# Kernel tuning notes

Measured on AMD Instinct MI355X. Metric: run time of the kernel, lower is better.

Reference implementation:

```python
import jax, jax.numpy as jnp
import numpy as np
import math

D_MODEL = 2048
NUM_HEADS = 32
NUM_KV_HEADS = 8
D_K = D_MODEL // NUM_HEADS  # 64
GROUPS = NUM_HEADS // NUM_KV_HEADS  # 4
WINDOW = 512
ROPE_BASE = 10000.0


def setup_inputs() -> dict:
    key = jax.random.key(0)
    ks = jax.random.split(key, 5)
    B, T = 2, 2048
    x = jax.random.normal(ks[0], (B, T, D_MODEL), dtype=jnp.float32)
    s = 0.02  # typical init scale to keep logits sane
    Wq = jax.random.normal(ks[1], (D_MODEL, D_MODEL), dtype=jnp.float32) * s
    Wk = jax.random.normal(ks[2], (NUM_KV_HEADS * D_K, D_MODEL), dtype=jnp.float32) * s
    Wv = jax.random.normal(ks[3], (NUM_KV_HEADS * D_K, D_MODEL), dtype=jnp.float32) * s
    Wo = jax.random.normal(ks[4], (D_MODEL, D_MODEL), dtype=jnp.float32) * s
    return {"x": x, "Wq": Wq, "Wk": Wk, "Wv": Wv, "Wo": Wo}


def _rotate_half(t):
    half = t.shape[-1] // 2
    return jnp.concatenate([-t[..., half:], t[..., :half]], axis=-1)


def _rope_cos_sin(T, dtype):
    inv_freq = 1.0 / (ROPE_BASE ** (jnp.arange(0, D_K, 2, dtype=jnp.float32) / D_K))
    pos = jnp.arange(T, dtype=jnp.float32)
    freqs = pos[:, None] * inv_freq[None, :]            # [T, D_K/2]
    emb = jnp.concatenate([freqs, freqs], axis=-1)       # [T, D_K]
    return jnp.cos(emb).astype(dtype)[None, None], jnp.sin(emb).astype(dtype)[None, None]


def reference(x, Wq, Wk, Wv, Wo):
    B, T, D = x.shape
    # Projections (nn.Linear: x @ W.T)
    Q = (x @ Wq.T).reshape(B, T, NUM_HEADS, D_K).transpose(0, 2, 1, 3)     # [B,H,T,dk]
    K = (x @ Wk.T).reshape(B, T, NUM_KV_HEADS, D_K).transpose(0, 2, 1, 3)  # [B,KV,T,dk]
    V = (x @ Wv.T).reshape(B, T, NUM_KV_HEADS, D_K).transpose(0, 2, 1, 3)
    # RoPE
    cos, sin = _rope_cos_sin(T, x.dtype)
    Q = Q * cos + _rotate_half(Q) * sin
    K = K * cos + _rotate_half(K) * sin
    # GQA: fold group dim into Q instead of repeat_interleave on K/V (same math)
    Qg = Q.reshape(B, NUM_KV_HEADS, GROUPS, T, D_K)
    scale = math.sqrt(D_K)
    scores = jnp.einsum('bhgqd,bhkd->bhgqk', Qg, K) / scale  # [B,KV,G,T,T]
    # sliding-window causal mask: valid iff 0 <= q_pos - k_pos < WINDOW
    pos = jnp.arange(T)
    dist = pos[:, None] - pos[None, :]
    win_mask = (dist < 0) | (dist >= WINDOW)
    scores = jnp.where(win_mask[None, None, None], -jnp.inf, scores)
    attn = jax.nn.softmax(scores, axis=-1)
    out = jnp.einsum('bhgqk,bhkd->bhgqd', attn, V)
    out = out.reshape(B, NUM_HEADS, T, D_K).transpose(0, 2, 1, 3).reshape(B, T, D)
    return out @ Wo.T
```

## Files before the change

kernel.cpp:

```cpp
#include <hip/hip_runtime.h>
#include <hip/hip_bf16.h>
#include <cstdint>
#include <cstddef>

typedef __attribute__((ext_vector_type(4))) float f32x4;
typedef __attribute__((ext_vector_type(8))) short bf16x8;
typedef __attribute__((ext_vector_type(4))) int i32x4;
typedef void __attribute__((address_space(1)))* as1_void_p;
typedef void __attribute__((address_space(3)))* as3_void_p;

#define T_SEQ 2048
#define D_MODEL 2048
#define NUM_HEADS 32
#define NUM_KV 8
#define GROUPS 4
#define DK 64
#define WINDOW 512
#define BATCH 2

#define NEG_BIG (-30000.0f)

__device__ __forceinline__ unsigned short f2b(float f) {
    unsigned int u = __builtin_bit_cast(unsigned int, f);
    u = (u + 0x7FFFu + ((u >> 16) & 1u)) >> 16;
    return (unsigned short)u;
}

__device__ __forceinline__ unsigned int cvtpk_bf16(float lo, float hi) {
    unsigned int r;
    asm("v_cvt_pk_bf16_f32 %0, %1, %2" : "=v"(r) : "v"(lo), "v"(hi));
    return r;
}

__device__ __forceinline__ void load_lds16(const void* g, void* l) {
    __builtin_amdgcn_global_load_lds((as1_void_p)(uintptr_t)g,
                                     (as3_void_p)(unsigned int)(uintptr_t)l,
                                     16, 0, 0);
}

#define CAST_N0 8388608
#define CAST_N1 12582912
#define CAST_N2 13631488
#define CAST_N3 14680064
#define CAST_N4 18874368
__global__ void cast_all_kernel(const float* __restrict__ x, const float* __restrict__ wq,
                                const float* __restrict__ wk, const float* __restrict__ wv,
                                const float* __restrict__ wo, unsigned short* __restrict__ dst) {
    int i = (blockIdx.x * blockDim.x + threadIdx.x) * 4;
    const int stride = gridDim.x * blockDim.x * 4;
    for (; i < CAST_N4; i += stride) {
        const float* src;
        int off;
        if (i < CAST_N0)      { src = x;  off = i; }
        else if (i < CAST_N1) { src = wq; off = i - CAST_N0; }
        else if (i < CAST_N2) { src = wk; off = i - CAST_N1; }
        else if (i < CAST_N3) { src = wv; off = i - CAST_N2; }
        else                  { src = wo; off = i - CAST_N3; }
        const float4 v = *(const float4*)(src + off);
        ushort4 o;
        o.x = f2b(v.x); o.y = f2b(v.y); o.z = f2b(v.z); o.w = f2b(v.w);
        *(ushort4*)(dst + i) = o;
    }
}

__global__ void rope_table_kernel(float* __restrict__ ct, float* __restrict__ st) {
    int i = blockIdx.x * blockDim.x + threadIdx.x;
    int t = i >> 5, j = i & 31;
    const float kln = 0.28782313662425556f;
    float inv = __expf(-(float)j * kln);
    if (j == 0) inv = 1.0f;
    float ang = (float)t * inv;
    float s, c;
    sincosf(ang, &s, &c);
    ct[i] = c; st[i] = s;
}


__global__ __launch_bounds__(512, 4) void gemm_qkv_rope(
    const unsigned short* __restrict__ A, const unsigned short* __restrict__ Bw,
    const float* __restrict__ ct, const float* __restrict__ st,
    unsigned short* __restrict__ Qb, unsigned short* __restrict__ Kb,
    unsigned short* __restrict__ Vt) {
    __shared__ __align__(16) unsigned short lds[32768];
    const int tid = threadIdx.x;
    const int lane = tid & 63;
    const int wid = tid >> 6;
    const int wr = wid >> 1, wc = wid & 1;
    const int lrow = lane & 15;
    const int g = lane >> 4;
    const int tile_m = blockIdx.y, tile_n = blockIdx.x;
    const int arow = tile_m * 128, brow = tile_n * 128;

    const int srow = tid >> 2, sslot = tid & 3;
    const int scol = (sslot ^ ((srow >> 1) & 3)) << 3;

    f32x4 acc[2][4] = {};

#define QSTAGE(BUF, KCOL)                                                      \
    {                                                                          \
        load_lds16(A + (size_t)(arow + srow) * 2048 + (KCOL) + scol,           \
                   (char*)&lds[(BUF) * 8192] + tid * 16);                      \
        load_lds16(Bw + (size_t)(brow + srow) * 2048 + (KCOL) + scol,          \
                   (char*)&lds[(BUF) * 8192 + 4096] + tid * 16);               \
    }

    QSTAGE(0, 0) QSTAGE(1, 32) QSTAGE(2, 64)
    asm volatile("s_waitcnt vmcnt(4)" ::: "memory");
    __builtin_amdgcn_sched_barrier(0);
    __builtin_amdgcn_s_barrier();

    for (int t = 0; t < 64; ++t) {
        const int cb = (t & 3) * 8192;
        const int sb = (t + 3) & 3;
        bf16x8 af[2], bfr[4];
#pragma unroll
        for (int m = 0; m < 2; ++m) {
            const int R = wr * 32 + m * 16 + lrow;
            af[m] = *(const bf16x8*)&lds[cb + R * 32 + ((g ^ ((R >> 1) & 3)) << 3)];
        }
#pragma unroll
        for (int n = 0; n < 4; ++n) {
            const int R = wc * 64 + n * 16 + lrow;
            bfr[n] = *(const bf16x8*)&lds[cb + 4096 + R * 32 + ((g ^ ((R >> 1) & 3)) << 3)];
        }
        if (t + 3 < 64) QSTAGE(sb, (t + 3) * 32)
        __builtin_amdgcn_s_barrier();
        asm volatile("s_waitcnt lgkmcnt(0)" ::: "memory");
        __builtin_amdgcn_sched_barrier(0);
        __builtin_amdgcn_s_setprio(1);
#pragma unroll
        for (int m = 0; m < 2; ++m)
#pragma unroll
            for (int n = 0; n < 4; ++n)
                acc[m][n] = __builtin_amdgcn_mfma_f32_16x16x32_bf16(af[m], bfr[n], acc[m][n], 0, 0, 0);
        __builtin_amdgcn_s_setprio(0);
        if (t < 63) { asm volatile("s_waitcnt vmcnt(4)" ::: "memory"); }
        else        { asm volatile("s_waitcnt vmcnt(0)" ::: "memory"); }
        __builtin_amdgcn_sched_barrier(0);
        __builtin_amdgcn_s_barrier();
    }
#undef QSTAGE

    const int hcol = tile_n * 2 + wc;
#pragma unroll
    for (int m = 0; m < 2; ++m) {
        const int row0 = tile_m * 128 + wr * 32 + m * 16 + g * 4;
        const int bb = row0 >> 11;
        const int t0 = row0 & 2047;
        if (hcol < 40) {
            const bool isQ = (hcol < 32);
            const float sc = isQ ? 0.125f : 1.0f;
            unsigned short* base = isQ
                ? (Qb + ((size_t)(bb * NUM_HEADS + hcol) * T_SEQ) * 64)
                : (Kb + ((size_t)(bb * NUM_KV + (hcol - 32)) * T_SEQ) * 64);
#pragma unroll
            for (int r = 0; r < 4; ++r) {
                const int t = t0 + r;
                unsigned short* dst = base + (size_t)t * 64;
#pragma unroll
                for (int n = 0; n < 2; ++n) {
                    const int j = n * 16 + lrow;
                    const float c = ct[t * 32 + j], s = st[t * 32 + j];
                    const float v0 = acc[m][n][r], v1 = acc[m][n + 2][r];
                    dst[j]      = f2b((v0 * c - v1 * s) * sc);
                    dst[j + 32] = f2b((v1 * c + v0 * s) * sc);
                }
            }
        } else {
            const int vh = hcol - 40;
            const int chunk = t0 >> 5, tk = t0 & 31;
            unsigned short* cbase = Vt + ((size_t)(bb * NUM_KV + vh) * 64 + chunk) * 2048 + tk;
#pragma unroll
            for (int n = 0; n < 4; ++n) {
                const int d = n * 16 + lrow;
                unsigned int u0 = cvtpk_bf16(acc[m][n][0], acc[m][n][1]);
                unsigned int u1 = cvtpk_bf16(acc[m][n][2], acc[m][n][3]);
                uint2 val; val.x = u0; val.y = u1;
                *(uint2*)(cbase + d * 32) = val;
            }
        }
    }
}

__global__ __launch_bounds__(512, 2) void gemm_bf16_nt(
    const unsigned short* __restrict__ A, const unsigned short* __restrict__ B,
    float* __restrict__ C) {
    __shared__ __align__(16) unsigned short lds[49152];
    const int tid = threadIdx.x;
    const int lane = tid & 63;
    const int wid = tid >> 6;
    const int wr = wid >> 2, wc = wid & 3;
    const int lrow = lane & 15;
    const int g = lane >> 4;
    const int tile_m = blockIdx.y, tile_n = blockIdx.x;
    const int arow = tile_m * 128, brow = tile_n * 256;

    const int srow = tid >> 2, sslot = tid & 3;
    const int scol = (sslot ^ ((srow >> 1) & 3)) << 3;

    f32x4 acc[4][4] = {};

#define OSTAGE(BUF, KCOL)                                                      \
    {                                                                          \
        load_lds16(A + (size_t)(arow + srow) * 2048 + (KCOL) + scol,           \
                   (char*)&lds[(BUF) * 12288] + tid * 16);                     \
        _Pragma("unroll") for (int u = 0; u < 2; ++u) {                        \
            const int gi = u * 512 + tid;                                      \
            const int br_ = gi >> 2, bs_ = gi & 3;                             \
            const int bc_ = (bs_ ^ ((br_ >> 1) & 3)) << 3;                     \
            load_lds16(B + (size_t)(brow + br_) * 2048 + (KCOL) + bc_,         \
                       (char*)&lds[(BUF) * 12288 + 4096] + gi * 16);           \
        }                                                                      \
    }

    OSTAGE(0, 0) OSTAGE(1, 32) OSTAGE(2, 64)
    asm volatile("s_waitcnt vmcnt(6)" ::: "memory");
    __builtin_amdgcn_sched_barrier(0);
    __builtin_amdgcn_s_barrier();

    for (int t = 0; t < 64; ++t) {
        const int cb = (t & 3) * 12288;
        const int sb = (t + 3) & 3;
        bf16x8 af[4], bfr[4];
#pragma unroll
        for (int m = 0; m < 4; ++m) {
            const int R = wr * 64 + m * 16 + lrow;
            af[m] = *(const bf16x8*)&lds[cb + R * 32 + ((g ^ ((R >> 1) & 3)) << 3)];
        }
#pragma unroll
        for (int n = 0; n < 4; ++n) {
            const int R = wc * 64 + n * 16 + lrow;
            bfr[n] = *(const bf16x8*)&lds[cb + 4096 + R * 32 + ((g ^ ((R >> 1) & 3)) << 3)];
        }
        if (t + 3 < 64) OSTAGE(sb, (t + 3) * 32)
        __builtin_amdgcn_s_barrier();
        asm volatile("s_waitcnt lgkmcnt(0)" ::: "memory");
        __builtin_amdgcn_sched_barrier(0);
        __builtin_amdgcn_s_setprio(1);
#pragma unroll
        for (int m = 0; m < 4; ++m)
#pragma unroll
            for (int n = 0; n < 4; ++n)
                acc[m][n] = __builtin_amdgcn_mfma_f32_16x16x32_bf16(af[m], bfr[n], acc[m][n], 0, 0, 0);
        __builtin_amdgcn_s_setprio(0);
        if (t < 63) { asm volatile("s_waitcnt vmcnt(6)" ::: "memory"); }
        else        { asm volatile("s_waitcnt vmcnt(0)" ::: "memory"); }
        __builtin_amdgcn_sched_barrier(0);
        __builtin_amdgcn_s_barrier();
    }
#undef OSTAGE

#pragma unroll
    for (int m = 0; m < 4; ++m)
#pragma unroll
        for (int n = 0; n < 4; ++n) {
            const int col = tile_n * 256 + wc * 64 + n * 16 + lrow;
#pragma unroll
            for (int r = 0; r < 4; ++r) {
                const int row = tile_m * 128 + wr * 64 + m * 16 + g * 4 + r;
                C[(size_t)row * 2048 + col] = acc[m][n][r];
            }
        }
}

__global__ __launch_bounds__(512, 2) void attn_kernel(
    const unsigned short* __restrict__ Qb, const unsigned short* __restrict__ Kb,
    const unsigned short* __restrict__ Vt, unsigned short* __restrict__ Oout) {
    __shared__ __align__(16) unsigned short lds[12288];
    const int tid = threadIdx.x;
    const int lane = tid & 63;
    const int wv = tid >> 6;
    const int g4 = wv & 3;
    const int tile = wv >> 2;
    const int bid = blockIdx.x;
    const int kvh = bid & 7;
    const int b = (bid >> 3) & 1;
    const int band = 63 - (bid >> 4);
    const int q0A = band * 32;
    const int q0w = q0A + tile * 16;
    const int h = kvh * 4 + g4;

    const int lq = lane & 15;
    const int g = lane >> 4;
    const int kq8 = g * 8;
    const int q = q0w + lq;

    const unsigned short* Qrow = Qb + ((size_t)((b * NUM_HEADS + h) * T_SEQ) + q) * 64;
    const bf16x8 qf0 = *(const bf16x8*)(Qrow + kq8);
    const bf16x8 qf1 = *(const bf16x8*)(Qrow + 32 + kq8);

    f32x4 acc[4] = {};
    float lrun = 0.0f;

    int kc_lo = q0A - (WINDOW - 1);
    if (kc_lo < 0) kc_lo = 0;
    kc_lo &= ~31;
    const int N = ((q0A - kc_lo) >> 5) + 1;

    const unsigned short* Kg = Kb + (size_t)(b * NUM_KV + kvh) * T_SEQ * 64
                                  + (size_t)kc_lo * 64;
    const unsigned short* Vg = Vt + (size_t)(b * NUM_KV + kvh) * 64 * T_SEQ
                                  + (size_t)(kc_lo >> 5) * 2048;

    const int perm = (lq >> 2) * 8 + (lq & 3);
#define SWZK(r) (((r & 3) | ((r >> 3) << 2)) & 7)
    const int koff0 = perm * 64 + ((g ^ SWZK(perm)) << 3);
    const int koff1 = perm * 64 + (((4 + g) ^ SWZK(perm)) << 3);
    const int perm4 = perm + 4;
    const int koff2 = perm4 * 64 + ((g ^ SWZK(perm4)) << 3);
    const int koff3 = perm4 * 64 + (((4 + g) ^ SWZK(perm4)) << 3);
    int voff[4];
#pragma unroll
    for (int nd = 0; nd < 4; ++nd)
        voff[nd] = 2048 + (nd * 16 + lq) * 32 + ((g ^ ((lq >> 1) & 3)) << 3);

#define STAGE(T, BUF)                                                          \
    {                                                                          \
        if (tid < 256) {                                                       \
            const int row_ = tid >> 3, ps = tid & 7;                           \
            const int ls = ps ^ SWZK(row_);                                    \
            load_lds16(Kg + (size_t)(T) * 2048 + row_ * 64 + ls * 8,           \
                       (char*)lds + (BUF) * 8192 + tid * 16);                  \
        } else {                                                               \
            const int gi = tid - 256;                                          \
            const int row_ = gi >> 2, ps = gi & 3;                             \
            const int ls = ps ^ ((row_ >> 1) & 3);                             \
            load_lds16(Vg + (size_t)(T) * 2048 + row_ * 32 + ls * 8,           \
                       (char*)lds + (BUF) * 8192 + 4096 + gi * 16);            \
        }                                                                      \
    }

    STAGE(0, 0)
    if (N > 1) {
        STAGE(1, 1)
        asm volatile("s_waitcnt vmcnt(1)" ::: "memory");
    } else {
        asm volatile("s_waitcnt vmcnt(0)" ::: "memory");
    }
    __builtin_amdgcn_sched_barrier(0);
    __builtin_amdgcn_s_barrier();

    int kb = 0;
    int sbuf = 2;
    for (int t = 0; t < N; ++t) {
        bf16x8 kf[4], vf[4];
        kf[0] = *(const bf16x8*)&lds[kb + koff0];
        kf[1] = *(const bf16x8*)&lds[kb + koff1];
        kf[2] = *(const bf16x8*)&lds[kb + koff2];
        kf[3] = *(const bf16x8*)&lds[kb + koff3];
#pragma unroll
        for (int nd = 0; nd < 4; ++nd) vf[nd] = *(const bf16x8*)&lds[kb + voff[nd]];
        if (t + 2 < N) STAGE(t + 2, sbuf)
        asm volatile("s_waitcnt lgkmcnt(0)" ::: "memory");
        __builtin_amdgcn_sched_barrier(0);

        const int kc = kc_lo + t * 32;
        f32x4 st2[2] = {};
        st2[0] = __builtin_amdgcn_mfma_f32_16x16x32_bf16(kf[0], qf0, st2[0], 0, 0, 0);
        st2[0] = __builtin_amdgcn_mfma_f32_16x16x32_bf16(kf[1], qf1, st2[0], 0, 0, 0);
        st2[1] = __builtin_amdgcn_mfma_f32_16x16x32_bf16(kf[2], qf0, st2[1], 0, 0, 0);
        st2[1] = __builtin_amdgcn_mfma_f32_16x16x32_bf16(kf[3], qf1, st2[1], 0, 0, 0);

        float s8[8];
#pragma unroll
        for (int tt = 0; tt < 2; ++tt)
#pragma unroll
            for (int r = 0; r < 4; ++r) s8[tt * 4 + r] = st2[tt][r];

        if (kc < q0w - 496 || kc > q0w - 31) {
#pragma unroll
            for (int i = 0; i < 8; ++i) {
                const int key = kc + g * 8 + ((i >> 2) << 2) + (i & 3);
                const int dist = q - key;
                if (dist < 0 || dist >= WINDOW) s8[i] = NEG_BIG;
            }
        }

        float p8[8];
        float ps = 0.0f;
#pragma unroll
        for (int i = 0; i < 8; ++i) {
            p8[i] = __expf(s8[i]);
            ps += p8[i];
        }
        lrun += ps;

        i32x4 pwi;
        pwi[0] = (int)cvtpk_bf16(p8[0], p8[1]);
        pwi[1] = (int)cvtpk_bf16(p8[2], p8[3]);
        pwi[2] = (int)cvtpk_bf16(p8[4], p8[5]);
        pwi[3] = (int)cvtpk_bf16(p8[6], p8[7]);
        const bf16x8 pw = __builtin_bit_cast(bf16x8, pwi);

#pragma unroll
        for (int nd = 0; nd < 4; ++nd)
            acc[nd] = __builtin_amdgcn_mfma_f32_16x16x32_bf16(vf[nd], pw, acc[nd], 0, 0, 0);

        if (t + 1 < N) {
            if (t + 2 < N) { asm volatile("s_waitcnt vmcnt(1)" ::: "memory"); }
            else           { asm volatile("s_waitcnt vmcnt(0)" ::: "memory"); }
            __builtin_amdgcn_sched_barrier(0);
            __builtin_amdgcn_s_barrier();
        }
        kb += 4096; if (kb == 12288) kb = 0;
        sbuf += 1;  if (sbuf == 3) sbuf = 0;
    }
#undef STAGE
#undef SWZK

    lrun += __shfl_xor(lrun, 16);
    lrun += __shfl_xor(lrun, 32);

    const float inv = 1.0f / lrun;
#pragma unroll
    for (int nd = 0; nd < 4; ++nd) {
        unsigned int u0 = cvtpk_bf16(acc[nd][0] * inv, acc[nd][1] * inv);
        unsigned int u1 = cvtpk_bf16(acc[nd][2] * inv, acc[nd][3] * inv);
        unsigned short* dst = Oout + ((size_t)(b * T_SEQ + q)) * D_MODEL + h * 64 + nd * 16 + g * 4;
        uint2 val; val.x = u0; val.y = u1;
        *(uint2*)dst = val;
    }
}

extern "C" void kernel_launch(void* const* d_in, const int* in_sizes, int n_in,
                              void* d_out, int out_size, void* d_ws, size_t ws_size,
                              hipStream_t stream) {
    const float* x = (const float*)d_in[0];
    const float* Wq = (const float*)d_in[1];
    const float* Wk = (const float*)d_in[2];
    const float* Wv = (const float*)d_in[3];
    const float* Wo = (const float*)d_in[4];
    float* out = (float*)d_out;

    char* ws = (char*)d_ws;
    size_t off = 0;
    auto alloc = [&](size_t bytes) -> char* {
        char* p = ws + off;
        off += (bytes + 255) & ~(size_t)255;
        return p;
    };
    unsigned short* xb   = (unsigned short*)alloc(8388608ull * 2);
    unsigned short* wcat = (unsigned short*)alloc(6291456ull * 2);
    unsigned short* wob  = (unsigned short*)alloc(4194304ull * 2);
    unsigned short* qb   = (unsigned short*)alloc(8388608ull * 2);
    unsigned short* kb   = (unsigned short*)alloc(2097152ull * 2);
    unsigned short* vt   = (unsigned short*)alloc(2097152ull * 2);
    unsigned short* attn = (unsigned short*)alloc(8388608ull * 2);
    float* ct            = (float*)alloc(65536ull * 4);
    float* st            = (float*)alloc(65536ull * 4);

    cast_all_kernel<<<2048, 256, 0, stream>>>(x, Wq, Wk, Wv, Wo, xb);
    rope_table_kernel<<<256, 256, 0, stream>>>(ct, st);

    gemm_qkv_rope<<<dim3(24, 32), 512, 0, stream>>>(xb, wcat, ct, st, qb, kb, vt);

    attn_kernel<<<1024, 512, 0, stream>>>(qb, kb, vt, attn);

    gemm_bf16_nt<<<dim3(8, 32), 512, 0, stream>>>(attn, wob, out);
}
```

Before: 155.4 us.

## Unify both GEMMs on a 4-wave 128x128 tile with 64x64 per-wave subtiles

Replaces the two GEMM main loops with one shared core. It uses 256-thread blocks, each wave computing a 64x64 sub-tile, with a 4-stage LDS ring for a 128x128 block tile. The QKV GEMM gives each wave more output per fragment load, improving register-level reuse. The output projection drops from a 128x256 tile to 128x128, doubling the block count to fill the CUs better. The cost is more accumulator registers per wave, fewer waves per block to hide latency, and more redundant global loads for the output GEMM.

```diff
diff --git a/kernel.cpp b/kernel.cpp
--- a/kernel.cpp
+++ b/kernel.cpp
@@ -76,75 +76,71 @@
 }
 
 
-__global__ __launch_bounds__(512, 4) void gemm_qkv_rope(
+#define GSTAGE(SRC, ROWBASE, KCOL, BYTEOFF)                                    \
+    { _Pragma("unroll") for (int u = 0; u < 2; ++u) {                          \
+        const int gi = u * 256 + tid;                                          \
+        const int row_ = gi >> 2, sl_ = gi & 3;                                \
+        const int sc_ = (sl_ ^ ((row_ >> 1) & 3)) << 3;                        \
+        load_lds16(SRC + (size_t)((ROWBASE) + row_) * 2048 + (KCOL) + sc_,     \
+                   (char*)lds + (BYTEOFF) + gi * 16); } }
+
+#define GEMM4_CORE(APTR, BPTR)                                                 \
+    const int tid = threadIdx.x;                                               \
+    const int lane = tid & 63;                                                 \
+    const int wid = tid >> 6;                                                  \
+    const int wr = wid >> 1, wc = wid & 1;                        \
+    const int lrow = lane & 15;                                                \
+    const int g = lane >> 4;                                                   \
+    const int tile_m = blockIdx.y, tile_n = blockIdx.x;                        \
+    const int arow = tile_m * 128, brow = tile_n * 128;                        \
+    f32x4 acc[4][4] = {};                                                      \
+    GSTAGE(APTR, arow, 0,  0)     GSTAGE(BPTR, brow, 0,  8192)                 \
+    GSTAGE(APTR, arow, 32, 16384) GSTAGE(BPTR, brow, 32, 24576)                \
+    GSTAGE(APTR, arow, 64, 32768) GSTAGE(BPTR, brow, 64, 40960)                \
+    asm volatile("s_waitcnt vmcnt(8)" ::: "memory");                           \
+    __builtin_amdgcn_sched_barrier(0);                                         \
+    __builtin_amdgcn_s_barrier();                                              \
+    for (int t = 0; t < 64; ++t) {                                             \
+        const int cb = (t & 3) * 8192;                         \
+        const int sbyte = ((t + 3) & 3) * 16384;                               \
+        bf16x8 af[4], bfr[4];                                                  \
+        _Pragma("unroll") for (int m = 0; m < 4; ++m) {                        \
+            const int R = wr * 64 + m * 16 + lrow;                             \
+            af[m] = *(const bf16x8*)&lds[cb + R * 32 + ((g ^ ((R >> 1) & 3)) << 3)]; \
+        }                                                                      \
+        _Pragma("unroll") for (int n = 0; n < 4; ++n) {                        \
+            const int R = wc * 64 + n * 16 + lrow;                             \
+            bfr[n] = *(const bf16x8*)&lds[cb + 4096 + R * 32 + ((g ^ ((R >> 1) & 3)) << 3)]; \
+        }                                                                      \
+        if (t + 3 < 64) {                                                      \
+            GSTAGE(APTR, arow, (t + 3) * 32, sbyte)                            \
+            GSTAGE(BPTR, brow, (t + 3) * 32, sbyte + 8192)                     \
+        }                                                                      \
+        asm volatile("s_waitcnt lgkmcnt(0)" ::: "memory");                     \
+        __builtin_amdgcn_sched_barrier(0);                                     \
+        __builtin_amdgcn_s_setprio(1);                                         \
+        _Pragma("unroll") for (int m = 0; m < 4; ++m)                          \
+            _Pragma("unroll") for (int n = 0; n < 4; ++n)                      \
+                acc[m][n] = __builtin_amdgcn_mfma_f32_16x16x32_bf16(af[m], bfr[n], acc[m][n], 0, 0, 0); \
+        __builtin_amdgcn_s_setprio(0);                                         \
+        if (t < 60) { asm volatile("s_waitcnt vmcnt(8)" ::: "memory"); }       \
+        else        { asm volatile("s_waitcnt vmcnt(0)" ::: "memory"); }       \
+        __builtin_amdgcn_sched_barrier(0);                                     \
+        __builtin_amdgcn_s_barrier();                                          \
+    }
+
+__global__ __launch_bounds__(256, 2) void gemm_qkv_rope(
     const unsigned short* __restrict__ A, const unsigned short* __restrict__ Bw,
     const float* __restrict__ ct, const float* __restrict__ st,
     unsigned short* __restrict__ Qb, unsigned short* __restrict__ Kb,
     unsigned short* __restrict__ Vt) {
     __shared__ __align__(16) unsigned short lds[32768];
-    const int tid = threadIdx.x;
-    const int lane = tid & 63;
-    const int wid = tid >> 6;
-    const int wr = wid >> 1, wc = wid & 1;
-    const int lrow = lane & 15;
-    const int g = lane >> 4;
-    const int tile_m = blockIdx.y, tile_n = blockIdx.x;
-    const int arow = tile_m * 128, brow = tile_n * 128;
-
-    const int srow = tid >> 2, sslot = tid & 3;
-    const int scol = (sslot ^ ((srow >> 1) & 3)) << 3;
-
-    f32x4 acc[2][4] = {};
-
-#define QSTAGE(BUF, KCOL)                                                      \
-    {                                                                          \
-        load_lds16(A + (size_t)(arow + srow) * 2048 + (KCOL) + scol,           \
-                   (char*)&lds[(BUF) * 8192] + tid * 16);                      \
-        load_lds16(Bw + (size_t)(brow + srow) * 2048 + (KCOL) + scol,          \
-                   (char*)&lds[(BUF) * 8192 + 4096] + tid * 16);               \
-    }
-
-    QSTAGE(0, 0) QSTAGE(1, 32) QSTAGE(2, 64)
-    asm volatile("s_waitcnt vmcnt(4)" ::: "memory");
-    __builtin_amdgcn_sched_barrier(0);
-    __builtin_amdgcn_s_barrier();
-
-    for (int t = 0; t < 64; ++t) {
-        const int cb = (t & 3) * 8192;
-        const int sb = (t + 3) & 3;
-        bf16x8 af[2], bfr[4];
-#pragma unroll
-        for (int m = 0; m < 2; ++m) {
-            const int R = wr * 32 + m * 16 + lrow;
-            af[m] = *(const bf16x8*)&lds[cb + R * 32 + ((g ^ ((R >> 1) & 3)) << 3)];
-        }
-#pragma unroll
-        for (int n = 0; n < 4; ++n) {
-            const int R = wc * 64 + n * 16 + lrow;
-            bfr[n] = *(const bf16x8*)&lds[cb + 4096 + R * 32 + ((g ^ ((R >> 1) & 3)) << 3)];
-        }
-        if (t + 3 < 64) QSTAGE(sb, (t + 3) * 32)
-        __builtin_amdgcn_s_barrier();
-        asm volatile("s_waitcnt lgkmcnt(0)" ::: "memory");
-        __builtin_amdgcn_sched_barrier(0);
-        __builtin_amdgcn_s_setprio(1);
-#pragma unroll
-        for (int m = 0; m < 2; ++m)
-#pragma unroll
-            for (int n = 0; n < 4; ++n)
-                acc[m][n] = __builtin_amdgcn_mfma_f32_16x16x32_bf16(af[m], bfr[n], acc[m][n], 0, 0, 0);
-        __builtin_amdgcn_s_setprio(0);
-        if (t < 63) { asm volatile("s_waitcnt vmcnt(4)" ::: "memory"); }
-        else        { asm volatile("s_waitcnt vmcnt(0)" ::: "memory"); }
-        __builtin_amdgcn_sched_barrier(0);
-        __builtin_amdgcn_s_barrier();
-    }
-#undef QSTAGE
+    GEMM4_CORE(A, Bw)
 
     const int hcol = tile_n * 2 + wc;
 #pragma unroll
-    for (int m = 0; m < 2; ++m) {
-        const int row0 = tile_m * 128 + wr * 32 + m * 16 + g * 4;
+    for (int m = 0; m < 4; ++m) {
+        const int row0 = tile_m * 128 + wr * 64 + m * 16 + g * 4;
         const int bb = row0 >> 11;
         const int t0 = row0 & 2047;
         if (hcol < 40) {
@@ -182,79 +178,17 @@
     }
 }
 
-__global__ __launch_bounds__(512, 2) void gemm_bf16_nt(
+__global__ __launch_bounds__(256, 2) void gemm_bf16_nt(
     const unsigned short* __restrict__ A, const unsigned short* __restrict__ B,
     float* __restrict__ C) {
-    __shared__ __align__(16) unsigned short lds[49152];
-    const int tid = threadIdx.x;
-    const int lane = tid & 63;
-    const int wid = tid >> 6;
-    const int wr = wid >> 2, wc = wid & 3;
-    const int lrow = lane & 15;
-    const int g = lane >> 4;
-    const int tile_m = blockIdx.y, tile_n = blockIdx.x;
-    const int arow = tile_m * 128, brow = tile_n * 256;
-
-    const int srow = tid >> 2, sslot = tid & 3;
-    const int scol = (sslot ^ ((srow >> 1) & 3)) << 3;
-
-    f32x4 acc[4][4] = {};
-
-#define OSTAGE(BUF, KCOL)                                                      \
-    {                                                                          \
-        load_lds16(A + (size_t)(arow + srow) * 2048 + (KCOL) + scol,           \
-                   (char*)&lds[(BUF) * 12288] + tid * 16);                     \
-        _Pragma("unroll") for (int u = 0; u < 2; ++u) {                        \
-            const int gi = u * 512 + tid;                                      \
-            const int br_ = gi >> 2, bs_ = gi & 3;                             \
-            const int bc_ = (bs_ ^ ((br_ >> 1) & 3)) << 3;                     \
-            load_lds16(B + (size_t)(brow + br_) * 2048 + (KCOL) + bc_,         \
-                       (char*)&lds[(BUF) * 12288 + 4096] + gi * 16);           \
-        }                                                                      \
-    }
-
-    OSTAGE(0, 0) OSTAGE(1, 32) OSTAGE(2, 64)
-    asm volatile("s_waitcnt vmcnt(6)" ::: "memory");
-    __builtin_amdgcn_sched_barrier(0);
-    __builtin_amdgcn_s_barrier();
-
-    for (int t = 0; t < 64; ++t) {
-        const int cb = (t & 3) * 12288;
-        const int sb = (t + 3) & 3;
-        bf16x8 af[4], bfr[4];
-#pragma unroll
-        for (int m = 0; m < 4; ++m) {
-            const int R = wr * 64 + m * 16 + lrow;
-            af[m] = *(const bf16x8*)&lds[cb + R * 32 + ((g ^ ((R >> 1) & 3)) << 3)];
-        }
+    __shared__ __align__(16) unsigned short lds[32768];
+    GEMM4_CORE(A, B)
+
+#pragma unroll
+    for (int m = 0; m < 4; ++m)
 #pragma unroll
         for (int n = 0; n < 4; ++n) {
-            const int R = wc * 64 + n * 16 + lrow;
-            bfr[n] = *(const bf16x8*)&lds[cb + 4096 + R * 32 + ((g ^ ((R >> 1) & 3)) << 3)];
-        }
-        if (t + 3 < 64) OSTAGE(sb, (t + 3) * 32)
-        __builtin_amdgcn_s_barrier();
-        asm volatile("s_waitcnt lgkmcnt(0)" ::: "memory");
-        __builtin_amdgcn_sched_barrier(0);
-        __builtin_amdgcn_s_setprio(1);
-#pragma unroll
-        for (int m = 0; m < 4; ++m)
-#pragma unroll
-            for (int n = 0; n < 4; ++n)
-                acc[m][n] = __builtin_amdgcn_mfma_f32_16x16x32_bf16(af[m], bfr[n], acc[m][n], 0, 0, 0);
-        __builtin_amdgcn_s_setprio(0);
-        if (t < 63) { asm volatile("s_waitcnt vmcnt(6)" ::: "memory"); }
-        else        { asm volatile("s_waitcnt vmcnt(0)" ::: "memory"); }
-        __builtin_amdgcn_sched_barrier(0);
-        __builtin_amdgcn_s_barrier();
-    }
-#undef OSTAGE
-
-#pragma unroll
-    for (int m = 0; m < 4; ++m)
-#pragma unroll
-        for (int n = 0; n < 4; ++n) {
-            const int col = tile_n * 256 + wc * 64 + n * 16 + lrow;
+            const int col = tile_n * 128 + wc * 64 + n * 16 + lrow;
 #pragma unroll
             for (int r = 0; r < 4; ++r) {
                 const int row = tile_m * 128 + wr * 64 + m * 16 + g * 4 + r;
@@ -452,9 +386,9 @@
     cast_all_kernel<<<2048, 256, 0, stream>>>(x, Wq, Wk, Wv, Wo, xb);
     rope_table_kernel<<<256, 256, 0, stream>>>(ct, st);
 
-    gemm_qkv_rope<<<dim3(24, 32), 512, 0, stream>>>(xb, wcat, ct, st, qb, kb, vt);
+    gemm_qkv_rope<<<dim3(24, 32), 256, 0, stream>>>(xb, wcat, ct, st, qb, kb, vt);
 
     attn_kernel<<<1024, 512, 0, stream>>>(qb, kb, vt, attn);
 
-    gemm_bf16_nt<<<dim3(8, 32), 512, 0, stream>>>(attn, wob, out);
-}
+    gemm_bf16_nt<<<dim3(16, 32), 256, 0, stream>>>(attn, wob, out);
+}
```

Result: slower. 160.9 us (+3.5%).
